# Optimization experiments

Hardware: AMD Instinct MI355X
Metric: run time of the kernel (lower is better)

The kernel has to match this reference:

```python
import jax, jax.numpy as jnp
import numpy as np

N_NODES = 100000
N_EDGES = 1600000
D_IN = 256
D_OUT = 64
BN_EPS = 1e-5


def setup_inputs() -> dict:
    key = jax.random.key(0)
    ks = jax.random.split(key, 8)
    x = jax.random.normal(ks[0], (N_NODES, D_IN), dtype=jnp.float32)
    edge_index = jax.random.randint(ks[1], (2, N_EDGES), 0, N_NODES, dtype=jnp.int32)
    W = jax.random.normal(ks[2], (D_OUT, D_IN), dtype=jnp.float32) / np.sqrt(D_IN).astype(np.float32)
    bias = 0.01 * jax.random.normal(ks[3], (D_OUT,), dtype=jnp.float32)
    gamma = 1.0 + 0.1 * jax.random.normal(ks[4], (D_OUT,), dtype=jnp.float32)
    beta = 0.1 * jax.random.normal(ks[5], (D_OUT,), dtype=jnp.float32)
    running_mean = 0.1 * jax.random.normal(ks[6], (D_OUT,), dtype=jnp.float32)
    running_var = jax.random.uniform(ks[7], (D_OUT,), dtype=jnp.float32, minval=0.5, maxval=1.5)
    return {"x": x, "edge_index": edge_index, "W": W, "bias": bias,
            "gamma": gamma, "beta": beta,
            "running_mean": running_mean, "running_var": running_var}


def reference(x, edge_index, W, bias, gamma, beta, running_mean, running_var):
    # GCNConv (PyG semantics): transform -> symmetric-normalized scatter-add with
    # self-loops (edge_weight = ones, self-loop weight = 1), then +bias.
    n = x.shape[0]
    loop = jnp.arange(n, dtype=edge_index.dtype)
    row = jnp.concatenate([edge_index[0], loop])  # source nodes
    col = jnp.concatenate([edge_index[1], loop])  # target nodes
    w = jnp.ones(row.shape[0], dtype=x.dtype)
    deg = jax.ops.segment_sum(w, col, num_segments=n)          # [N]
    dinv = jnp.where(deg > 0, jax.lax.rsqrt(deg), 0.0)          # D^{-1/2}
    norm = dinv[row] * w * dinv[col]                            # [E+N]
    xw = x @ W.T                                                # [N, D_OUT]
    agg = jax.ops.segment_sum(norm[:, None] * xw[row], col, num_segments=n)
    out = agg + bias
    # BatchNorm1d in eval mode (running stats); dropout inactive in eval.
    out = (out - running_mean) * jax.lax.rsqrt(running_var + BN_EPS) * gamma + beta
    return jax.nn.relu(out)
```

## Files before the change

### kernel.cpp

```cpp
#include <hip/hip_runtime.h>
#include <hip/hip_bf16.h>

#define D_IN 256
#define D_OUT 64
#define BN_EPS 1e-5f

#define BINSHIFT 8
#define BINCAP 4608
#define PCHUNK 8192

typedef __attribute__((ext_vector_type(4))) float floatx4;
typedef __attribute__((ext_vector_type(8))) __bf16 bf16x8;
typedef __attribute__((ext_vector_type(4))) unsigned uintx4;

__global__ __launch_bounds__(256) void k_prepart(
        const float* __restrict__ W, __bf16* __restrict__ whi, __bf16* __restrict__ wlo,
        const float* __restrict__ bias, const float* __restrict__ gamma,
        const float* __restrict__ beta, const float* __restrict__ rmean,
        const float* __restrict__ rvar,
        float* __restrict__ bnsc, float* __restrict__ bnsh,
        const int* __restrict__ ei, int* __restrict__ bincur,
        unsigned* __restrict__ pairs, int E, int nbins) {
    int b = blockIdx.x, t = threadIdx.x;
    if (b < 8) {
        int tid = b * 256 + t;
        int lane = tid & 63, c = (tid >> 6) & 7, tt = tid >> 9;
        int row = tt * 16 + (lane & 15);
        int k0 = c * 32 + (lane >> 4) * 8;
        size_t dst = (size_t)tid * 8;
        #pragma unroll
        for (int j = 0; j < 8; ++j) {
            float w = W[(size_t)row * D_IN + k0 + j];
            __bf16 h = (__bf16)w;
            whi[dst + j] = h;
            wlo[dst + j] = (__bf16)(w - (float)h);
        }
        return;
    }
    if (b == 8) {
        if (t < D_OUT) {
            float sc = rsqrtf(rvar[t] + BN_EPS) * gamma[t];
            bnsc[t] = sc;
            bnsh[t] = (bias[t] - rmean[t]) * sc + beta[t];
        }
        return;
    }

    __shared__ int hist[512];
    __shared__ int base[512];
    int e0 = (b - 9) * PCHUNK;

    for (int j = t; j < nbins; j += 256) hist[j] = 0;
    __syncthreads();

    int cols[PCHUNK / 256];
    int rows[PCHUNK / 256];
    int ranks[PCHUNK / 256];
    #pragma unroll
    for (int i = 0; i < PCHUNK / 256; ++i) {
        int e = e0 + i * 256 + t;
        if (e < E) {
            int c = ei[E + e];
            cols[i] = c;
            rows[i] = ei[e];
            ranks[i] = atomicAdd(&hist[c >> BINSHIFT], 1);
        }
    }
    __syncthreads();
    for (int j = t; j < nbins; j += 256)
        base[j] = atomicAdd(&bincur[j], hist[j]);
    __syncthreads();
    #pragma unroll
    for (int i = 0; i < PCHUNK / 256; ++i) {
        int e = e0 + i * 256 + t;
        if (e < E) {
            int c = cols[i];
            int bin = c >> BINSHIFT;
            int pos = base[bin] + ranks[i];
            if (pos >= BINCAP) pos = BINCAP - 1;
            pairs[(size_t)bin * BINCAP + pos] =
                ((unsigned)rows[i] << 8) | (unsigned)(c & 255);
        }
    }
}

__global__ __launch_bounds__(256) void k_fill3(
        const unsigned* __restrict__ pairs, const int* __restrict__ bincur,
        int* __restrict__ off, float* __restrict__ dinv,
        int* __restrict__ srcs, int n, int nbins) {
    __shared__ int hist[256];
    __shared__ int sc[256];
    __shared__ int nbase[256];
    __shared__ int sbase;
    int bin = blockIdx.x, t = threadIdx.x;

    int i0 = 2 * t, i1 = 2 * t + 1;
    int v0 = (i0 < nbins) ? bincur[i0] : 0;
    int v1 = (i1 < nbins) ? bincur[i1] : 0;
    int s = v0 + v1;
    sc[t] = s;
    hist[t] = 0;
    __syncthreads();
    for (int o = 1; o < 256; o <<= 1) {
        int v = (t >= o) ? sc[t - o] : 0;
        __syncthreads();
        sc[t] += v;
        __syncthreads();
    }
    int excl = sc[t] - s;
    if (t == (bin >> 1)) sbase = (bin & 1) ? (excl + v0) : excl;
    if (bin == 0 && t == 255) off[n] = sc[255];
    __syncthreads();
    int binoff_b = sbase;

    int cnt = bincur[bin]; if (cnt > BINCAP) cnt = BINCAP;
    const unsigned* bp = pairs + (size_t)bin * BINCAP;
    unsigned vals[BINCAP / 256];
    int rks[BINCAP / 256];
    #pragma unroll
    for (int i = 0; i < BINCAP / 256; ++i) {
        int p = t + i * 256;
        if (p < cnt) {
            unsigned v = bp[p];
            vals[i] = v;
            rks[i] = atomicAdd(&hist[v & 255u], 1);
        }
    }
    __syncthreads();
    int own = hist[t];
    sc[t] = own;
    __syncthreads();
    for (int o = 1; o < 256; o <<= 1) {
        int v = (t >= o) ? sc[t - o] : 0;
        __syncthreads();
        sc[t] += v;
        __syncthreads();
    }
    int base = binoff_b + sc[t] - own;
    nbase[t] = base;
    int node = (bin << BINSHIFT) + t;
    if (node < n) {
        off[node] = base;
        dinv[node] = rsqrtf((float)(own + 1));
    }
    __syncthreads();
    #pragma unroll
    for (int i = 0; i < BINCAP / 256; ++i) {
        int p = t + i * 256;
        if (p < cnt) {
            unsigned v = vals[i];
            srcs[nbase[v & 255u] + rks[i]] = (int)(v >> 8);
        }
    }
}

__global__ __launch_bounds__(256) void k_gemm(
        const float* __restrict__ x, const __bf16* __restrict__ whi,
        const __bf16* __restrict__ wlo, const float* __restrict__ dinv,
        __bf16* __restrict__ yb, int n) {
    int wave = threadIdx.x >> 6;
    int lane = threadIdx.x & 63;
    int m0 = blockIdx.x * 64 + wave * 16;
    if (m0 >= n) return;
    int q = lane >> 4, cl = lane & 15;
    int arow = m0 + cl; if (arow >= n) arow = n - 1;
    const float* ap = x + (size_t)arow * D_IN + q * 8;

    floatx4 acc[4] = {{0.f,0.f,0.f,0.f},{0.f,0.f,0.f,0.f},
                      {0.f,0.f,0.f,0.f},{0.f,0.f,0.f,0.f}};

    #pragma unroll
    for (int c = 0; c < 8; ++c) {
        floatx4 a0 = *(const floatx4*)(ap + c * 32);
        floatx4 a1 = *(const floatx4*)(ap + c * 32 + 4);
        bf16x8 ahi, alo;
        #pragma unroll
        for (int j = 0; j < 4; ++j) {
            __bf16 h0 = (__bf16)a0[j];
            __bf16 h1 = (__bf16)a1[j];
            ahi[j] = h0;     alo[j] = (__bf16)(a0[j] - (float)h0);
            ahi[4 + j] = h1; alo[4 + j] = (__bf16)(a1[j] - (float)h1);
        }
        #pragma unroll
        for (int t = 0; t < 4; ++t) {
            size_t fo = ((size_t)(t * 8 + c) * 64 + lane) * 8;
            bf16x8 bh = *(const bf16x8*)(whi + fo);
            bf16x8 bl = *(const bf16x8*)(wlo + fo);
            acc[t] = __builtin_amdgcn_mfma_f32_16x16x32_bf16(ahi, bh, acc[t], 0, 0, 0);
            acc[t] = __builtin_amdgcn_mfma_f32_16x16x32_bf16(alo, bh, acc[t], 0, 0, 0);
            acc[t] = __builtin_amdgcn_mfma_f32_16x16x32_bf16(ahi, bl, acc[t], 0, 0, 0);
        }
    }

    int nb = m0 + q * 4;
    float dv[4];
    #pragma unroll
    for (int r = 0; r < 4; ++r) dv[r] = (nb + r < n) ? dinv[nb + r] : 0.f;
    #pragma unroll
    for (int t = 0; t < 4; ++t) {
        #pragma unroll
        for (int r = 0; r < 4; ++r) {
            int node = nb + r;
            if (node < n)
                yb[(size_t)node * D_OUT + t * 16 + cl] = (__bf16)(dv[r] * acc[t][r]);
        }
    }
}

__device__ __forceinline__ void acc_row4(uintx4 v, float (&a)[8]) {
    #pragma unroll
    for (int k = 0; k < 4; ++k) {
        a[2 * k]     += __uint_as_float(v[k] << 16);
        a[2 * k + 1] += __uint_as_float(v[k] & 0xffff0000u);
    }
}

__global__ __launch_bounds__(256) void k_aggregate(
        const int* __restrict__ off, const int* __restrict__ srcs,
        const unsigned* __restrict__ ybf, const float* __restrict__ dinv,
        const float* __restrict__ bnsc, const float* __restrict__ bnsh,
        float* __restrict__ out, int n) {
    int node = blockIdx.x * 4 + (threadIdx.x >> 6);
    if (node >= n) return;
    int lane = threadIdx.x & 63;
    int g = lane >> 3, sl = lane & 7;
    int s = off[node], e2 = off[node + 1];

    float a[8] = {0.f, 0.f, 0.f, 0.f, 0.f, 0.f, 0.f, 0.f};
    float dv = 0.f;
    floatx4 bs0, bs1, bh0, bh1;
    if (g == 0) {
        dv = dinv[node];
        bs0 = *(const floatx4*)(bnsc + sl * 8);
        bs1 = *(const floatx4*)(bnsc + sl * 8 + 4);
        bh0 = *(const floatx4*)(bnsh + sl * 8);
        bh1 = *(const floatx4*)(bnsh + sl * 8 + 4);
        uintx4 v = *(const uintx4*)(ybf + (size_t)node * 32 + sl * 4);
        acc_row4(v, a);
    }

    int e = s + g;
    for (; e + 24 < e2; e += 32) {
        int r0 = srcs[e], r1 = srcs[e + 8], r2 = srcs[e + 16], r3 = srcs[e + 24];
        uintx4 v0 = *(const uintx4*)(ybf + (size_t)r0 * 32 + sl * 4);
        uintx4 v1 = *(const uintx4*)(ybf + (size_t)r1 * 32 + sl * 4);
        uintx4 v2 = *(const uintx4*)(ybf + (size_t)r2 * 32 + sl * 4);
        uintx4 v3 = *(const uintx4*)(ybf + (size_t)r3 * 32 + sl * 4);
        acc_row4(v0, a);
        acc_row4(v1, a);
        acc_row4(v2, a);
        acc_row4(v3, a);
    }
    for (; e + 8 < e2; e += 16) {
        int r0 = srcs[e], r1 = srcs[e + 8];
        uintx4 v0 = *(const uintx4*)(ybf + (size_t)r0 * 32 + sl * 4);
        uintx4 v1 = *(const uintx4*)(ybf + (size_t)r1 * 32 + sl * 4);
        acc_row4(v0, a);
        acc_row4(v1, a);
    }
    for (; e < e2; e += 8) {
        uintx4 v = *(const uintx4*)(ybf + (size_t)srcs[e] * 32 + sl * 4);
        acc_row4(v, a);
    }

    #pragma unroll
    for (int k = 0; k < 8; ++k) {
        a[k] += __shfl_xor(a[k], 8);
        a[k] += __shfl_xor(a[k], 16);
        a[k] += __shfl_xor(a[k], 32);
    }

    if (g == 0) {
        float o[8];
        #pragma unroll
        for (int k = 0; k < 4; ++k) {
            o[k]     = fmaf(dv * a[k],     bs0[k], bh0[k]);
            o[4 + k] = fmaf(dv * a[4 + k], bs1[k], bh1[k]);
        }
        floatx4 w0 = { fmaxf(o[0], 0.f), fmaxf(o[1], 0.f),
                       fmaxf(o[2], 0.f), fmaxf(o[3], 0.f) };
        floatx4 w1 = { fmaxf(o[4], 0.f), fmaxf(o[5], 0.f),
                       fmaxf(o[6], 0.f), fmaxf(o[7], 0.f) };
        *(floatx4*)(out + (size_t)node * D_OUT + sl * 8) = w0;
        *(floatx4*)(out + (size_t)node * D_OUT + sl * 8 + 4) = w1;
    }
}

static inline char* align_up(char* p, size_t a) {
    return (char*)(((uintptr_t)p + a - 1) & ~(uintptr_t)(a - 1));
}

extern "C" void kernel_launch(void* const* d_in, const int* in_sizes, int n_in,
                              void* d_out, int out_size, void* d_ws, size_t ws_size,
                              hipStream_t stream) {
    const float* x     = (const float*)d_in[0];
    const int*   ei    = (const int*)d_in[1];
    const float* W     = (const float*)d_in[2];
    const float* bias  = (const float*)d_in[3];
    const float* gamma = (const float*)d_in[4];
    const float* beta  = (const float*)d_in[5];
    const float* rmean = (const float*)d_in[6];
    const float* rvar  = (const float*)d_in[7];
    float* out = (float*)d_out;

    int N = in_sizes[0] / D_IN;
    int E = in_sizes[1] / 2;
    int nbins = (N + (1 << BINSHIFT) - 1) >> BINSHIFT;
    int nchunks = (E + PCHUNK - 1) / PCHUNK;

    char* p = (char*)d_ws;
    int*      bincur = (int*)p;         p += 512 * 4;
    int*      off    = (int*)p;         p += (size_t)(N + 1) * 4; p = align_up(p, 256);
    float*    dinv   = (float*)p;       p += (size_t)N * 4;       p = align_up(p, 256);
    float*    bnsc   = (float*)p;       p += D_OUT * 4;
    float*    bnsh   = (float*)p;       p += D_OUT * 4;           p = align_up(p, 256);
    __bf16*   whi    = (__bf16*)p;      p += (size_t)D_OUT * D_IN * 2; p = align_up(p, 256);
    __bf16*   wlo    = (__bf16*)p;      p += (size_t)D_OUT * D_IN * 2; p = align_up(p, 256);
    __bf16*   yb     = (__bf16*)p;      p += (size_t)N * D_OUT * 2;    p = align_up(p, 256);
    int*      srcs   = (int*)p;         p += (size_t)E * 4;       p = align_up(p, 256);
    unsigned* pairs  = (unsigned*)p;

    hipMemsetAsync(bincur, 0, 512 * 4, stream);
    k_prepart<<<9 + nchunks, 256, 0, stream>>>(W, whi, wlo, bias, gamma, beta,
                                               rmean, rvar, bnsc, bnsh,
                                               ei, bincur, pairs, E, nbins);
    k_fill3<<<nbins, 256, 0, stream>>>(pairs, bincur, off, dinv, srcs, N, nbins);
    k_gemm<<<(N + 63) / 64, 256, 0, stream>>>(x, whi, wlo, dinv, yb, N);
    k_aggregate<<<(N + 3) / 4, 256, 0, stream>>>(off, srcs, (const unsigned*)yb,
                                                 dinv, bnsc, bnsh, out, N);
}
```

Baseline: 275.8 us.

## Merge CSR fill and GEMM into one launch using global degree atomics

Degree counting moves into the partition kernel through global atomicAdd on a per-node deg array, so the GEMM no longer waits for the fill kernel to produce dinv. The bin-fill blocks and the GEMM blocks then run in a single launch and overlap. This removes one kernel launch and the serial dependency between them. In exchange it adds 1.6M global atomics and a larger memset, and rsqrt is recomputed from deg in both consumers.

```diff
diff --git a/kernel.cpp b/kernel.cpp
--- a/kernel.cpp
+++ b/kernel.cpp
@@ -19,7 +19,7 @@
         const float* __restrict__ beta, const float* __restrict__ rmean,
         const float* __restrict__ rvar,
         float* __restrict__ bnsc, float* __restrict__ bnsh,
-        const int* __restrict__ ei, int* __restrict__ bincur,
+        const int* __restrict__ ei, int* __restrict__ bincur, int* __restrict__ deg,
         unsigned* __restrict__ pairs, int E, int nbins) {
     int b = blockIdx.x, t = threadIdx.x;
     if (b < 8) {
@@ -64,6 +64,7 @@
             cols[i] = c;
             rows[i] = ei[e];
             ranks[i] = atomicAdd(&hist[c >> BINSHIFT], 1);
+            atomicAdd(&deg[c], 1);
         }
     }
     __syncthreads();
@@ -84,15 +85,71 @@
     }
 }
 
-__global__ __launch_bounds__(256) void k_fill3(
+__global__ __launch_bounds__(256) void k_fillgemm(
         const unsigned* __restrict__ pairs, const int* __restrict__ bincur,
-        int* __restrict__ off, float* __restrict__ dinv,
-        int* __restrict__ srcs, int n, int nbins) {
+        int* __restrict__ off, int* __restrict__ srcs,
+        const float* __restrict__ x, const __bf16* __restrict__ whi,
+        const __bf16* __restrict__ wlo, const int* __restrict__ deg,
+        __bf16* __restrict__ yb, int n, int nbins) {
     __shared__ int hist[256];
     __shared__ int sc[256];
     __shared__ int nbase[256];
     __shared__ int sbase;
-    int bin = blockIdx.x, t = threadIdx.x;
+    int b = blockIdx.x, t = threadIdx.x;
+
+    if (b >= nbins) {
+        int wave = t >> 6;
+        int lane = t & 63;
+        int m0 = (b - nbins) * 64 + wave * 16;
+        if (m0 >= n) return;
+        int q = lane >> 4, cl = lane & 15;
+        int arow = m0 + cl; if (arow >= n) arow = n - 1;
+        const float* ap = x + (size_t)arow * D_IN + q * 8;
+
+        floatx4 acc[4] = {{0.f,0.f,0.f,0.f},{0.f,0.f,0.f,0.f},
+                          {0.f,0.f,0.f,0.f},{0.f,0.f,0.f,0.f}};
+
+        #pragma unroll
+        for (int c = 0; c < 8; ++c) {
+            floatx4 a0 = *(const floatx4*)(ap + c * 32);
+            floatx4 a1 = *(const floatx4*)(ap + c * 32 + 4);
+            bf16x8 ahi, alo;
+            #pragma unroll
+            for (int j = 0; j < 4; ++j) {
+                __bf16 h0 = (__bf16)a0[j];
+                __bf16 h1 = (__bf16)a1[j];
+                ahi[j] = h0;     alo[j] = (__bf16)(a0[j] - (float)h0);
+                ahi[4 + j] = h1; alo[4 + j] = (__bf16)(a1[j] - (float)h1);
+            }
+            #pragma unroll
+            for (int u = 0; u < 4; ++u) {
+                size_t fo = ((size_t)(u * 8 + c) * 64 + lane) * 8;
+                bf16x8 bh = *(const bf16x8*)(whi + fo);
+                bf16x8 bl = *(const bf16x8*)(wlo + fo);
+                acc[u] = __builtin_amdgcn_mfma_f32_16x16x32_bf16(ahi, bh, acc[u], 0, 0, 0);
+                acc[u] = __builtin_amdgcn_mfma_f32_16x16x32_bf16(alo, bh, acc[u], 0, 0, 0);
+                acc[u] = __builtin_amdgcn_mfma_f32_16x16x32_bf16(ahi, bl, acc[u], 0, 0, 0);
+            }
+        }
+
+        int nb = m0 + q * 4;
+        float dv[4];
+        #pragma unroll
+        for (int r = 0; r < 4; ++r)
+            dv[r] = (nb + r < n) ? rsqrtf((float)(deg[nb + r] + 1)) : 0.f;
+        #pragma unroll
+        for (int u = 0; u < 4; ++u) {
+            #pragma unroll
+            for (int r = 0; r < 4; ++r) {
+                int node = nb + r;
+                if (node < n)
+                    yb[(size_t)node * D_OUT + u * 16 + cl] = (__bf16)(dv[r] * acc[u][r]);
+            }
+        }
+        return;
+    }
+
+    int bin = b;
 
     int i0 = 2 * t, i1 = 2 * t + 1;
     int v0 = (i0 < nbins) ? bincur[i0] : 0;
@@ -139,10 +196,7 @@
     int base = binoff_b + sc[t] - own;
     nbase[t] = base;
     int node = (bin << BINSHIFT) + t;
-    if (node < n) {
-        off[node] = base;
-        dinv[node] = rsqrtf((float)(own + 1));
-    }
+    if (node < n) off[node] = base;
     __syncthreads();
     #pragma unroll
     for (int i = 0; i < BINCAP / 256; ++i) {
@@ -154,59 +208,6 @@
     }
 }
 
-__global__ __launch_bounds__(256) void k_gemm(
-        const float* __restrict__ x, const __bf16* __restrict__ whi,
-        const __bf16* __restrict__ wlo, const float* __restrict__ dinv,
-        __bf16* __restrict__ yb, int n) {
-    int wave = threadIdx.x >> 6;
-    int lane = threadIdx.x & 63;
-    int m0 = blockIdx.x * 64 + wave * 16;
-    if (m0 >= n) return;
-    int q = lane >> 4, cl = lane & 15;
-    int arow = m0 + cl; if (arow >= n) arow = n - 1;
-    const float* ap = x + (size_t)arow * D_IN + q * 8;
-
-    floatx4 acc[4] = {{0.f,0.f,0.f,0.f},{0.f,0.f,0.f,0.f},
-                      {0.f,0.f,0.f,0.f},{0.f,0.f,0.f,0.f}};
-
-    #pragma unroll
-    for (int c = 0; c < 8; ++c) {
-        floatx4 a0 = *(const floatx4*)(ap + c * 32);
-        floatx4 a1 = *(const floatx4*)(ap + c * 32 + 4);
-        bf16x8 ahi, alo;
-        #pragma unroll
-        for (int j = 0; j < 4; ++j) {
-            __bf16 h0 = (__bf16)a0[j];
-            __bf16 h1 = (__bf16)a1[j];
-            ahi[j] = h0;     alo[j] = (__bf16)(a0[j] - (float)h0);
-            ahi[4 + j] = h1; alo[4 + j] = (__bf16)(a1[j] - (float)h1);
-        }
-        #pragma unroll
-        for (int t = 0; t < 4; ++t) {
-            size_t fo = ((size_t)(t * 8 + c) * 64 + lane) * 8;
-            bf16x8 bh = *(const bf16x8*)(whi + fo);
-            bf16x8 bl = *(const bf16x8*)(wlo + fo);
-            acc[t] = __builtin_amdgcn_mfma_f32_16x16x32_bf16(ahi, bh, acc[t], 0, 0, 0);
-            acc[t] = __builtin_amdgcn_mfma_f32_16x16x32_bf16(alo, bh, acc[t], 0, 0, 0);
-            acc[t] = __builtin_amdgcn_mfma_f32_16x16x32_bf16(ahi, bl, acc[t], 0, 0, 0);
-        }
-    }
-
-    int nb = m0 + q * 4;
-    float dv[4];
-    #pragma unroll
-    for (int r = 0; r < 4; ++r) dv[r] = (nb + r < n) ? dinv[nb + r] : 0.f;
-    #pragma unroll
-    for (int t = 0; t < 4; ++t) {
-        #pragma unroll
-        for (int r = 0; r < 4; ++r) {
-            int node = nb + r;
-            if (node < n)
-                yb[(size_t)node * D_OUT + t * 16 + cl] = (__bf16)(dv[r] * acc[t][r]);
-        }
-    }
-}
-
 __device__ __forceinline__ void acc_row4(uintx4 v, float (&a)[8]) {
     #pragma unroll
     for (int k = 0; k < 4; ++k) {
@@ -217,7 +218,7 @@
 
 __global__ __launch_bounds__(256) void k_aggregate(
         const int* __restrict__ off, const int* __restrict__ srcs,
-        const unsigned* __restrict__ ybf, const float* __restrict__ dinv,
+        const unsigned* __restrict__ ybf, const int* __restrict__ deg,
         const float* __restrict__ bnsc, const float* __restrict__ bnsh,
         float* __restrict__ out, int n) {
     int node = blockIdx.x * 4 + (threadIdx.x >> 6);
@@ -230,7 +231,7 @@
     float dv = 0.f;
     floatx4 bs0, bs1, bh0, bh1;
     if (g == 0) {
-        dv = dinv[node];
+        dv = rsqrtf((float)(deg[node] + 1));
         bs0 = *(const floatx4*)(bnsc + sl * 8);
         bs1 = *(const floatx4*)(bnsc + sl * 8 + 4);
         bh0 = *(const floatx4*)(bnsh + sl * 8);
@@ -310,8 +311,8 @@
 
     char* p = (char*)d_ws;
     int*      bincur = (int*)p;         p += 512 * 4;
+    int*      deg    = (int*)p;         p += (size_t)N * 4;       p = align_up(p, 256);
     int*      off    = (int*)p;         p += (size_t)(N + 1) * 4; p = align_up(p, 256);
-    float*    dinv   = (float*)p;       p += (size_t)N * 4;       p = align_up(p, 256);
     float*    bnsc   = (float*)p;       p += D_OUT * 4;
     float*    bnsh   = (float*)p;       p += D_OUT * 4;           p = align_up(p, 256);
     __bf16*   whi    = (__bf16*)p;      p += (size_t)D_OUT * D_IN * 2; p = align_up(p, 256);
@@ -320,12 +321,12 @@
     int*      srcs   = (int*)p;         p += (size_t)E * 4;       p = align_up(p, 256);
     unsigned* pairs  = (unsigned*)p;
 
-    hipMemsetAsync(bincur, 0, 512 * 4, stream);
+    hipMemsetAsync(bincur, 0, 512 * 4 + (size_t)N * 4, stream);
     k_prepart<<<9 + nchunks, 256, 0, stream>>>(W, whi, wlo, bias, gamma, beta,
                                                rmean, rvar, bnsc, bnsh,
-                                               ei, bincur, pairs, E, nbins);
-    k_fill3<<<nbins, 256, 0, stream>>>(pairs, bincur, off, dinv, srcs, N, nbins);
-    k_gemm<<<(N + 63) / 64, 256, 0, stream>>>(x, whi, wlo, dinv, yb, N);
+                                               ei, bincur, deg, pairs, E, nbins);
+    k_fillgemm<<<nbins + (N + 63) / 64, 256, 0, stream>>>(
+        pairs, bincur, off, srcs, x, whi, wlo, deg, yb, N, nbins);
     k_aggregate<<<(N + 3) / 4, 256, 0, stream>>>(off, srcs, (const unsigned*)yb,
-                                                 dinv, bnsc, bnsh, out, N);
-}
+                                                 deg, bnsc, bnsh, out, N);
+}
```

New measurement: 323.0 us. +17.1%, slower.
